# Optimization experiments

Hardware: AMD Instinct MI355X
Metric: run time of the kernel (lower is better)

## Reference

```python
import jax, jax.numpy as jnp
import numpy as np

N = 20000; E = 320000; IN = 128; OUT = 128; H = 8; D = 16
SQRT_DK = float(D) ** 0.5

def setup_inputs() -> dict:
    key = jax.random.key(0)
    ks = jax.random.split(key, 20)
    s = 0.05
    glorot = (6.0 / (D + D)) ** 0.5
    inp = dict(
        h_a=jax.random.normal(ks[0], (N, IN), jnp.float32),
        h_b=jax.random.normal(ks[1], (N, IN), jnp.float32),
        Wk=jax.random.normal(ks[2], (2, IN, OUT), jnp.float32) * s,
        bk=jnp.zeros((2, OUT), jnp.float32),
        Wq=jax.random.normal(ks[3], (2, IN, OUT), jnp.float32) * s,
        bq=jnp.zeros((2, OUT), jnp.float32),
        Wv=jax.random.normal(ks[4], (2, IN, OUT), jnp.float32) * s,
        bv=jnp.zeros((2, OUT), jnp.float32),
        Wa=jax.random.normal(ks[5], (2, OUT, OUT), jnp.float32) * s,
        ba=jnp.zeros((2, OUT), jnp.float32),
        rel_att=jax.random.normal(ks[6], (4, H, D, D), jnp.float32) * glorot,
        rel_msg=jax.random.normal(ks[7], (4, H, D, D), jnp.float32) * glorot,
        rel_pri=jnp.ones((4, H), jnp.float32),
        skip=jnp.ones((2,), jnp.float32),
    )
    names = ["src_aa", "dst_aa", "src_ab", "dst_ab", "src_ba", "dst_ba", "src_bb", "dst_bb"]
    for i, name in enumerate(names):
        inp[name] = jax.random.randint(ks[8 + i], (E,), 0, N, jnp.int32)
    return inp

def _relation(h_src, h_dst, src, dst, Wk_t, bk_t, Wq_t, bq_t, Wv_t, bv_t, att, msg, pri):
    # relation-specific K/V transform + Q projection
    k = (h_src @ Wk_t + bk_t).reshape(-1, H, D)
    v = (h_src @ Wv_t + bv_t).reshape(-1, H, D)
    q = (h_dst @ Wq_t + bq_t).reshape(-1, H, D)
    k = jnp.einsum('nhd,hde->nhe', k, att)
    v = jnp.einsum('nhd,hde->nhe', v, msg)
    # edge dot-product score (v_dot_u: q[dst] . k[src]), [E, H]
    score = jnp.einsum('ehd,ehd->eh', q[dst], k[src]) * pri / SQRT_DK
    # edge softmax normalized by dst
    smax = jax.ops.segment_max(score, dst, num_segments=N)
    ex = jnp.exp(score - smax[dst])
    ssum = jax.ops.segment_sum(ex, dst, num_segments=N)
    attn = ex / ssum[dst]
    # weighted scatter-aggregate, [N, H, D]
    return jax.ops.segment_sum(v[src] * attn[:, :, None], dst, num_segments=N)

def reference(h_a, h_b, Wk, bk, Wq, bq, Wv, bv, Wa, ba, rel_att, rel_msg, rel_pri, skip,
              src_aa, dst_aa, src_ab, dst_ab, src_ba, dst_ba, src_bb, dst_bb):
    agg_aa = _relation(h_a, h_a, src_aa, dst_aa, Wk[0], bk[0], Wq[0], bq[0], Wv[0], bv[0], rel_att[0], rel_msg[0], rel_pri[0])
    agg_ab = _relation(h_a, h_b, src_ab, dst_ab, Wk[0], bk[0], Wq[1], bq[1], Wv[0], bv[0], rel_att[1], rel_msg[1], rel_pri[1])
    agg_ba = _relation(h_b, h_a, src_ba, dst_ba, Wk[1], bk[1], Wq[0], bq[0], Wv[1], bv[1], rel_att[2], rel_msg[2], rel_pri[2])
    agg_bb = _relation(h_b, h_b, src_bb, dst_bb, Wk[1], bk[1], Wq[1], bq[1], Wv[1], bv[1], rel_att[3], rel_msg[3], rel_pri[3])
    # cross_reducer='mean' over the 2 relations targeting each node type
    t_a = (0.5 * (agg_aa + agg_ba)).reshape(N, OUT)
    t_b = (0.5 * (agg_ab + agg_bb)).reshape(N, OUT)
    al_a = jax.nn.sigmoid(skip[0])
    al_b = jax.nn.sigmoid(skip[1])
    new_a = al_a * (t_a @ Wa[0] + ba[0]) + (1.0 - al_a) * h_a
    new_b = al_b * (t_b @ Wa[1] + ba[1]) + (1.0 - al_b) * h_b
    return new_a, new_b
```

## Files before the change

kernel.cpp:

```cpp
#include <hip/hip_runtime.h>
#include <stdint.h>

#define N_NODES 20000
#define N_EDGES 320000
#define C 128
#define H 8
#define D 16
#define SLOT 64
#define NRANGE 5000
#define BUCKETS 2500
#define BCAP 224

#define P_CVT 2500
#define P_ZERO 157
#define P_PACK 128
#define P_FUSE 32
#define PB_EDGES 16384
#define PART_BLOCKS 80
#define PROJ_BLOCKS 3130
#define MB_TOTAL (PART_BLOCKS + PROJ_BLOCKS)

typedef short s16x8 __attribute__((ext_vector_type(8)));
typedef float f32x4 __attribute__((ext_vector_type(4)));

__device__ __forceinline__ unsigned short f2bf(float f) {
    unsigned int b = __float_as_uint(f);
    b += 0x7fffu + ((b >> 16) & 1u);
    return (unsigned short)(b >> 16);
}
__device__ __forceinline__ float bf2f(unsigned int u) {
    return __uint_as_float(u << 16);
}
__device__ __forceinline__ float bf_lo(unsigned int u) {
    return __uint_as_float(u << 16);
}
__device__ __forceinline__ float bf_hi(unsigned int u) {
    return __uint_as_float(u & 0xffff0000u);
}

__global__ __launch_bounds__(256) void prep_k(const float* __restrict__ h_a, const float* __restrict__ h_b,
                                              unsigned short* __restrict__ oa, unsigned short* __restrict__ ob,
                                              const float* __restrict__ Wq, const float* __restrict__ Wa,
                                              unsigned short* __restrict__ Wqt, unsigned short* __restrict__ Wat,
                                              const float* __restrict__ Wk, const float* __restrict__ Wv,
                                              const float* __restrict__ bk, const float* __restrict__ bv,
                                              const float* __restrict__ att, const float* __restrict__ msg,
                                              unsigned short* __restrict__ Wkt, unsigned short* __restrict__ Wvt,
                                              float* __restrict__ bkt, float* __restrict__ bvt,
                                              int* __restrict__ cur) {
    __shared__ float sa[D * D], sm[D * D];
    int bid = blockIdx.x;
    int tid = threadIdx.x;
    if (bid < P_CVT) {
        int i = (bid * 256 + tid) * 4;
        float4 va = *(const float4*)(h_a + i);
        float4 vb = *(const float4*)(h_b + i);
        ushort4 ua = { f2bf(va.x), f2bf(va.y), f2bf(va.z), f2bf(va.w) };
        ushort4 ub = { f2bf(vb.x), f2bf(vb.y), f2bf(vb.z), f2bf(vb.w) };
        *(ushort4*)(oa + i) = ua;
        *(ushort4*)(ob + i) = ub;
        return;
    }
    bid -= P_CVT;
    if (bid < P_ZERO) {
        int i = bid * 256 + tid;
        if (i < 40000) ((int4*)cur)[i] = make_int4(0, 0, 0, 0);
        return;
    }
    bid -= P_ZERO;
    if (bid < P_PACK) {
        int n = bid;
        int t = tid >> 7, i = tid & 127;
        Wqt[(t * C + n) * C + i] = f2bf(Wq[(t * C + i) * C + n]);
        Wat[(t * C + n) * C + i] = f2bf(Wa[(t * C + i) * C + n]);
        return;
    }
    bid -= P_PACK;
    {
        int r = bid >> 3, h = bid & 7;
        int t = r >> 1;
        if (tid < D * D) {
            sa[tid] = att[(r * H + h) * D * D + tid];
            sm[tid] = msg[(r * H + h) * D * D + tid];
        }
        __syncthreads();
        int i = tid & 127;
        for (int e = (tid >> 7); e < D; e += 2) {
            float sk = 0.f, sv = 0.f;
            for (int d = 0; d < D; ++d) {
                sk += Wk[(t * C + i) * C + h * D + d] * sa[d * D + e];
                sv += Wv[(t * C + i) * C + h * D + d] * sm[d * D + e];
            }
            Wkt[(r * C + h * D + e) * C + i] = f2bf(sk);
            Wvt[(r * C + h * D + e) * C + i] = f2bf(sv);
        }
        if (tid < D) {
            int e = tid;
            float sk = 0.f, sv = 0.f;
            for (int d = 0; d < D; ++d) {
                sk += bk[t * C + h * D + d] * sa[d * D + e];
                sv += bv[t * C + h * D + d] * sm[d * D + e];
            }
            bkt[r * C + h * D + e] = sk;
            bvt[r * C + h * D + e] = sv;
        }
    }
}

__global__ __launch_bounds__(256) void mega_k(const int* __restrict__ s0, const int* __restrict__ s1,
                                              const int* __restrict__ s2, const int* __restrict__ s3,
                                              const int* __restrict__ d0, const int* __restrict__ d1,
                                              const int* __restrict__ d2, const int* __restrict__ d3,
                                              int* __restrict__ cur, unsigned int* __restrict__ part,
                                              const unsigned short* __restrict__ ha,
                                              const unsigned short* __restrict__ hb,
                                              const unsigned short* __restrict__ Wqt,
                                              const unsigned short* __restrict__ Wkt,
                                              const unsigned short* __restrict__ Wvt,
                                              const float* __restrict__ bq,
                                              const float* __restrict__ bkt,
                                              const float* __restrict__ bvt,
                                              unsigned short* __restrict__ Qa,
                                              unsigned short* __restrict__ Qb,
                                              unsigned short* __restrict__ Kall,
                                              unsigned short* __restrict__ Vall) {
    __shared__ int hcnt[BUCKETS];
    __shared__ int hbase[BUCKETS];
    int bid = blockIdx.x;
    int tid = threadIdx.x;

    if (bid < PART_BLOCKS) {
        int r  = bid & 3;
        int pb = bid >> 2;
        int start = pb * PB_EDGES;
        int nval = N_EDGES - start;
        if (nval > PB_EDGES) nval = PB_EDGES;
        int nq = nval >> 2;
        const int* dd = (r == 0) ? d0 : (r == 1) ? d1 : (r == 2) ? d2 : d3;
        const int* ss = (r == 0) ? s0 : (r == 1) ? s1 : (r == 2) ? s2 : s3;
        for (int b = tid; b < BUCKETS; b += 256) hcnt[b] = 0;
        __syncthreads();
        for (int i = tid; i < nq; i += 256) {
            int4 d4 = *(const int4*)(dd + start + i * 4);
            atomicAdd(&hcnt[d4.x >> 3], 1);
            atomicAdd(&hcnt[d4.y >> 3], 1);
            atomicAdd(&hcnt[d4.z >> 3], 1);
            atomicAdd(&hcnt[d4.w >> 3], 1);
        }
        __syncthreads();
        for (int b = tid; b < BUCKETS; b += 256) {
            int c = hcnt[b];
            hbase[b] = c ? atomicAdd(&cur[(r * BUCKETS + b) * 16], c) : 0;
            hcnt[b] = 0;
        }
        __syncthreads();
        for (int i = tid; i < nq; i += 256) {
            int4 d4 = *(const int4*)(dd + start + i * 4);
            int4 s4 = *(const int4*)(ss + start + i * 4);
            int b0 = d4.x >> 3, b1 = d4.y >> 3, b2 = d4.z >> 3, b3 = d4.w >> 3;
            int i0 = atomicAdd(&hcnt[b0], 1);
            int i1 = atomicAdd(&hcnt[b1], 1);
            int i2 = atomicAdd(&hcnt[b2], 1);
            int i3 = atomicAdd(&hcnt[b3], 1);
            int p0 = hbase[b0] + i0, p1 = hbase[b1] + i1, p2 = hbase[b2] + i2, p3 = hbase[b3] + i3;
            if (p0 < BCAP) part[(size_t)(r * BUCKETS + b0) * BCAP + p0] = (unsigned int)s4.x | ((unsigned int)(d4.x & 7) << 15);
            if (p1 < BCAP) part[(size_t)(r * BUCKETS + b1) * BCAP + p1] = (unsigned int)s4.y | ((unsigned int)(d4.y & 7) << 15);
            if (p2 < BCAP) part[(size_t)(r * BUCKETS + b2) * BCAP + p2] = (unsigned int)s4.z | ((unsigned int)(d4.z & 7) << 15);
            if (p3 < BCAP) part[(size_t)(r * BUCKETS + b3) * BCAP + p3] = (unsigned int)s4.w | ((unsigned int)(d4.w & 7) << 15);
        }
        return;
    }
    int proj_id = bid - PART_BLOCKS;
    int j = proj_id / 313;
    int xb = proj_id - j * 313;
    const unsigned short* A;
    const unsigned short* Wt;
    const float* bias;
    unsigned short* Out;
    if (j < 2) {
        A = j ? hb : ha; Wt = Wqt + j * C * C; bias = bq + j * C; Out = j ? Qb : Qa;
    } else if (j < 6) {
        int r = j - 2;
        A = (r < 2) ? ha : hb; Wt = Wkt + r * C * C; bias = bkt + r * C;
        Out = Kall + (size_t)r * N_NODES * C;
    } else {
        int r = j - 6;
        A = (r < 2) ? ha : hb; Wt = Wvt + r * C * C; bias = bvt + r * C;
        Out = Vall + (size_t)r * N_NODES * C;
    }
    int wid = threadIdx.x >> 6, l = threadIdx.x & 63;
    int row_base = xb * 64 + wid * 16;
    int lm = l & 15, q = l >> 4;
    f32x4 acc[8] = {};
    int arow = row_base + lm;
    if (arow >= N_NODES) arow = N_NODES - 1;
    const s16x8* Ap = (const s16x8*)(A + (size_t)arow * C);
#pragma unroll
    for (int kc = 0; kc < 4; ++kc) {
        s16x8 af = Ap[kc * 4 + q];
#pragma unroll
        for (int t = 0; t < 8; ++t) {
            s16x8 bf = *(const s16x8*)(Wt + (t * 16 + lm) * C + kc * 32 + q * 8);
            acc[t] = __builtin_amdgcn_mfma_f32_16x16x32_bf16(af, bf, acc[t], 0, 0, 0);
        }
    }
#pragma unroll
    for (int t = 0; t < 8; ++t) {
        int col = t * 16 + lm;
        float b = bias[col];
#pragma unroll
        for (int i = 0; i < 4; ++i) {
            int row = row_base + q * 4 + i;
            if (row < N_NODES) Out[(size_t)row * C + col] = f2bf(acc[t][i] + b);
        }
    }
}

__global__ __launch_bounds__(256) void final_mm(const unsigned short* __restrict__ AggAll,
                                                const unsigned short* __restrict__ WatAll,
                                                const float* __restrict__ baAll,
                                                const float* __restrict__ skip,
                                                const float* __restrict__ h_a,
                                                const float* __restrict__ h_b,
                                                float* __restrict__ OutAll) {
    int ty = blockIdx.y;
    const unsigned short* Agg = AggAll + (size_t)ty * N_NODES * C;
    const unsigned short* Wat = WatAll + ty * C * C;
    const float* ba = baAll + ty * C;
    const float* h_orig = ty ? h_b : h_a;
    float* Out = OutAll + (size_t)ty * N_NODES * C;
    int wid = threadIdx.x >> 6, l = threadIdx.x & 63;
    int row_base = blockIdx.x * 64 + wid * 16;
    int lm = l & 15, q = l >> 4;
    f32x4 acc[8] = {};
    int arow = row_base + lm;
    if (arow >= N_NODES) arow = N_NODES - 1;
    const s16x8* Ap = (const s16x8*)(Agg + (size_t)arow * C);
#pragma unroll
    for (int kc = 0; kc < 4; ++kc) {
        s16x8 af = Ap[kc * 4 + q];
#pragma unroll
        for (int t = 0; t < 8; ++t) {
            s16x8 bf = *(const s16x8*)(Wat + (t * 16 + lm) * C + kc * 32 + q * 8);
            acc[t] = __builtin_amdgcn_mfma_f32_16x16x32_bf16(af, bf, acc[t], 0, 0, 0);
        }
    }
    float al = 1.f / (1.f + __expf(-skip[ty]));
#pragma unroll
    for (int t = 0; t < 8; ++t) {
        int col = t * 16 + lm;
        float b = ba[col];
#pragma unroll
        for (int i = 0; i < 4; ++i) {
            int row = row_base + q * 4 + i;
            if (row < N_NODES)
                Out[(size_t)row * C + col] = al * (acc[t][i] + b) + (1.f - al) * h_orig[(size_t)row * C + col];
        }
    }
}

__global__ __launch_bounds__(256) void node_p2(const int* __restrict__ cur,
                                               const unsigned int* __restrict__ part,
                                               const unsigned int* __restrict__ Kall,
                                               const unsigned int* __restrict__ Vall,
                                               const float* __restrict__ pri,
                                               const unsigned int* __restrict__ Qa,
                                               const unsigned int* __restrict__ Qb,
                                               unsigned int* __restrict__ agg) {
    __shared__ unsigned short slot[2][4][SLOT];
    __shared__ int cnt[2][4];
    int g = blockIdx.x;
    int xcd = g & 7, idx = g >> 3;
    int type = xcd >> 2;
    int range = (xcd & 3) * 1250 + idx;
    int relA = type ? 1 : 0;
    int relB = type ? 3 : 2;
    if (threadIdx.x < 8) ((int*)cnt)[threadIdx.x] = 0;
    __syncthreads();
    int bkt = range >> 1;
    int w   = range & 1;
#pragma unroll
    for (int rr = 0; rr < 2; ++rr) {
        int rel = rr ? relB : relA;
        int c = cur[(rel * BUCKETS + bkt) * 16];
        if (c > BCAP) c = BCAP;
        const unsigned int* pp = part + (size_t)(rel * BUCKETS + bkt) * BCAP;
        for (int i = threadIdx.x; i < c; i += 256) {
            unsigned int rec = pp[i];
            int dlow = (rec >> 15) & 7;
            if ((dlow >> 2) == w) {
                int dof = dlow & 3;
                int p = atomicAdd(&cnt[rr][dof], 1);
                if (p < SLOT) slot[rr][dof][p] = (unsigned short)(rec & 0x7fffu);
            }
        }
    }
    __syncthreads();

    int wid = threadIdx.x >> 6, l = threadIdx.x & 63;
    int eg = l >> 4;
    int j  = l & 15;
    int hg = j >> 1;
    int dof = wid;
    int n = range * 4 + dof;
    const unsigned int* Q32 = type ? Qb : Qa;
    uint4 qv = *(const uint4*)(Q32 + (size_t)n * 64 + j * 4);
    float q0 = bf_lo(qv.x), q1 = bf_hi(qv.x), q2 = bf_lo(qv.y), q3 = bf_hi(qv.y);
    float q4 = bf_lo(qv.z), q5 = bf_hi(qv.z), q6 = bf_lo(qv.w), q7 = bf_hi(qv.w);
    float out[8] = {};

#pragma unroll 1
    for (int rr = 0; rr < 2; ++rr) {
        int rel = rr ? relB : relA;
        const char* Kb = (const char*)(Kall + (size_t)rel * N_NODES * 64);
        const char* Vb = (const char*)(Vall + (size_t)rel * N_NODES * 64);
        float pv = pri[rel * 8 + hg] * 0.25f;
        int deg = cnt[rr][dof];
        if (deg > SLOT) deg = SLOT;
        float m = -1e30f, sum = 0.f;
        float acc[8] = {};
        for (int base = 0; base < deg; base += 16) {
            float s[4];
            uint4 vv[4];
#pragma unroll
            for (int i = 0; i < 4; ++i) {
                int idx2 = base + i * 4 + eg;
                float d = -1e30f;
                uint4 v = {0u, 0u, 0u, 0u};
                if (idx2 < deg) {
                    unsigned off = ((unsigned)slot[rr][dof][idx2] << 8) | ((unsigned)j << 4);
                    uint4 kv = *(const uint4*)(Kb + off);
                    v = *(const uint4*)(Vb + off);
                    d = q0 * bf_lo(kv.x) + q1 * bf_hi(kv.x)
                      + q2 * bf_lo(kv.y) + q3 * bf_hi(kv.y)
                      + q4 * bf_lo(kv.z) + q5 * bf_hi(kv.z)
                      + q6 * bf_lo(kv.w) + q7 * bf_hi(kv.w);
                    d += __shfl_xor(d, 1);
                    d *= pv;
                }
                s[i] = d;
                vv[i] = v;
            }
            float mloc = fmaxf(fmaxf(s[0], s[1]), fmaxf(s[2], s[3]));
            float mnew = fmaxf(m, mloc);
            float alpha = __expf(m - mnew);
            sum *= alpha;
#pragma unroll
            for (int c2 = 0; c2 < 8; ++c2) acc[c2] *= alpha;
            m = mnew;
#pragma unroll
            for (int i = 0; i < 4; ++i) {
                float ww = (s[i] > -1e29f) ? __expf(s[i] - m) : 0.f;
                sum += ww;
                acc[0] += ww * bf_lo(vv[i].x); acc[1] += ww * bf_hi(vv[i].x);
                acc[2] += ww * bf_lo(vv[i].y); acc[3] += ww * bf_hi(vv[i].y);
                acc[4] += ww * bf_lo(vv[i].z); acc[5] += ww * bf_hi(vv[i].z);
                acc[6] += ww * bf_lo(vv[i].w); acc[7] += ww * bf_hi(vv[i].w);
            }
        }
        float m1 = fmaxf(m, __shfl_xor(m, 16));
        float m2 = fmaxf(m1, __shfl_xor(m1, 32));
        float beta = __expf(m - m2);
        sum *= beta;
        sum += __shfl_xor(sum, 16);
        sum += __shfl_xor(sum, 32);
#pragma unroll
        for (int c2 = 0; c2 < 8; ++c2) {
            float a = acc[c2] * beta;
            a += __shfl_xor(a, 16);
            a += __shfl_xor(a, 32);
            acc[c2] = a;
        }
        if (deg > 0) {
            float rs = 1.f / sum;
#pragma unroll
            for (int c2 = 0; c2 < 8; ++c2) out[c2] += acc[c2] * rs;
        }
    }
    if (eg == 0) {
        uint4 pk;
        pk.x = (unsigned int)f2bf(0.5f * out[0]) | ((unsigned int)f2bf(0.5f * out[1]) << 16);
        pk.y = (unsigned int)f2bf(0.5f * out[2]) | ((unsigned int)f2bf(0.5f * out[3]) << 16);
        pk.z = (unsigned int)f2bf(0.5f * out[4]) | ((unsigned int)f2bf(0.5f * out[5]) << 16);
        pk.w = (unsigned int)f2bf(0.5f * out[6]) | ((unsigned int)f2bf(0.5f * out[7]) << 16);
        *(uint4*)(agg + ((size_t)type * N_NODES + n) * 64 + j * 4) = pk;
    }
}

extern "C" void kernel_launch(void* const* d_in, const int* in_sizes, int n_in,
                              void* d_out, int out_size, void* d_ws, size_t ws_size,
                              hipStream_t stream) {
    const float* h_a  = (const float*)d_in[0];
    const float* h_b  = (const float*)d_in[1];
    const float* Wk   = (const float*)d_in[2];
    const float* bk   = (const float*)d_in[3];
    const float* Wq   = (const float*)d_in[4];
    const float* bq   = (const float*)d_in[5];
    const float* Wv   = (const float*)d_in[6];
    const float* bv   = (const float*)d_in[7];
    const float* Wa   = (const float*)d_in[8];
    const float* ba   = (const float*)d_in[9];
    const float* att  = (const float*)d_in[10];
    const float* msg  = (const float*)d_in[11];
    const float* pri  = (const float*)d_in[12];
    const float* skip = (const float*)d_in[13];
    const int* srcs[4] = {(const int*)d_in[14], (const int*)d_in[16], (const int*)d_in[18], (const int*)d_in[20]};
    const int* dsts[4] = {(const int*)d_in[15], (const int*)d_in[17], (const int*)d_in[19], (const int*)d_in[21]};
    float* out = (float*)d_out;

    char* w = (char*)d_ws;
    auto alloc = [&](size_t bytes) {
        char* p = w;
        w += (bytes + 255) & ~(size_t)255;
        return p;
    };
    unsigned short* ha_bf = (unsigned short*)alloc((size_t)N_NODES * C * 2);
    unsigned short* hb_bf = (unsigned short*)alloc((size_t)N_NODES * C * 2);
    unsigned short* Qa    = (unsigned short*)alloc((size_t)N_NODES * C * 2);
    unsigned short* Qb    = (unsigned short*)alloc((size_t)N_NODES * C * 2);
    unsigned short* Kall  = (unsigned short*)alloc((size_t)4 * N_NODES * C * 2);
    unsigned short* Vall  = (unsigned short*)alloc((size_t)4 * N_NODES * C * 2);
    unsigned short* Wqt   = (unsigned short*)alloc(2 * C * C * 2);
    unsigned short* Wat   = (unsigned short*)alloc(2 * C * C * 2);
    unsigned short* Wkt   = (unsigned short*)alloc(4 * C * C * 2);
    unsigned short* Wvt   = (unsigned short*)alloc(4 * C * C * 2);
    float* bkt            = (float*)alloc(4 * C * 4);
    float* bvt            = (float*)alloc(4 * C * 4);
    int* cur              = (int*)alloc((size_t)4 * BUCKETS * 16 * 4);
    unsigned int* part    = (unsigned int*)alloc((size_t)4 * BUCKETS * BCAP * 4);
    unsigned short* agg   = (unsigned short*)alloc((size_t)2 * N_NODES * C * 2);

    prep_k<<<P_CVT + P_ZERO + P_PACK + P_FUSE, 256, 0, stream>>>(
        h_a, h_b, ha_bf, hb_bf, Wq, Wa, Wqt, Wat,
        Wk, Wv, bk, bv, att, msg, Wkt, Wvt, bkt, bvt, cur);

    mega_k<<<MB_TOTAL, 256, 0, stream>>>(
        srcs[0], srcs[1], srcs[2], srcs[3],
        dsts[0], dsts[1], dsts[2], dsts[3],
        cur, part,
        ha_bf, hb_bf, Wqt, Wkt, Wvt, bq, bkt, bvt,
        Qa, Qb, Kall, Vall);

    node_p2<<<2 * NRANGE, 256, 0, stream>>>(cur, part,
                                            (const unsigned int*)Kall, (const unsigned int*)Vall,
                                            pri,
                                            (const unsigned int*)Qa, (const unsigned int*)Qb,
                                            (unsigned int*)agg);

    final_mm<<<dim3(313, 2), 256, 0, stream>>>(agg, Wat, ba, skip, h_a, h_b, out);
}
```

Before: 307.7 us.

## Fuse final output projection and skip blend into node aggregation kernel

Removes the separate final_mm kernel and the bf16 aggregate buffer. Each node_p2 block keeps its four nodes' aggregated features in fp32 shared memory, then computes the Wa projection, bias, and sigmoid-weighted skip blend with scalar FMAs over bf16 weights. This saves a kernel launch and the aggregate round trip through global memory. In exchange, MFMA is replaced by scalar dot products, and each thread rereads 256-byte weight rows for every node.

```diff
diff --git a/kernel.cpp b/kernel.cpp
--- a/kernel.cpp
+++ b/kernel.cpp
@@ -216,49 +216,6 @@
     }
 }
 
-__global__ __launch_bounds__(256) void final_mm(const unsigned short* __restrict__ AggAll,
-                                                const unsigned short* __restrict__ WatAll,
-                                                const float* __restrict__ baAll,
-                                                const float* __restrict__ skip,
-                                                const float* __restrict__ h_a,
-                                                const float* __restrict__ h_b,
-                                                float* __restrict__ OutAll) {
-    int ty = blockIdx.y;
-    const unsigned short* Agg = AggAll + (size_t)ty * N_NODES * C;
-    const unsigned short* Wat = WatAll + ty * C * C;
-    const float* ba = baAll + ty * C;
-    const float* h_orig = ty ? h_b : h_a;
-    float* Out = OutAll + (size_t)ty * N_NODES * C;
-    int wid = threadIdx.x >> 6, l = threadIdx.x & 63;
-    int row_base = blockIdx.x * 64 + wid * 16;
-    int lm = l & 15, q = l >> 4;
-    f32x4 acc[8] = {};
-    int arow = row_base + lm;
-    if (arow >= N_NODES) arow = N_NODES - 1;
-    const s16x8* Ap = (const s16x8*)(Agg + (size_t)arow * C);
-#pragma unroll
-    for (int kc = 0; kc < 4; ++kc) {
-        s16x8 af = Ap[kc * 4 + q];
-#pragma unroll
-        for (int t = 0; t < 8; ++t) {
-            s16x8 bf = *(const s16x8*)(Wat + (t * 16 + lm) * C + kc * 32 + q * 8);
-            acc[t] = __builtin_amdgcn_mfma_f32_16x16x32_bf16(af, bf, acc[t], 0, 0, 0);
-        }
-    }
-    float al = 1.f / (1.f + __expf(-skip[ty]));
-#pragma unroll
-    for (int t = 0; t < 8; ++t) {
-        int col = t * 16 + lm;
-        float b = ba[col];
-#pragma unroll
-        for (int i = 0; i < 4; ++i) {
-            int row = row_base + q * 4 + i;
-            if (row < N_NODES)
-                Out[(size_t)row * C + col] = al * (acc[t][i] + b) + (1.f - al) * h_orig[(size_t)row * C + col];
-        }
-    }
-}
-
 __global__ __launch_bounds__(256) void node_p2(const int* __restrict__ cur,
                                                const unsigned int* __restrict__ part,
                                                const unsigned int* __restrict__ Kall,
@@ -266,9 +223,15 @@
                                                const float* __restrict__ pri,
                                                const unsigned int* __restrict__ Qa,
                                                const unsigned int* __restrict__ Qb,
-                                               unsigned int* __restrict__ agg) {
+                                               const unsigned short* __restrict__ WatAll,
+                                               const float* __restrict__ baAll,
+                                               const float* __restrict__ skip,
+                                               const float* __restrict__ h_a,
+                                               const float* __restrict__ h_b,
+                                               float* __restrict__ OutAll) {
     __shared__ unsigned short slot[2][4][SLOT];
     __shared__ int cnt[2][4];
+    __shared__ __align__(16) float aggl[4][C];
     int g = blockIdx.x;
     int xcd = g & 7, idx = g >> 3;
     int type = xcd >> 2;
@@ -378,12 +341,37 @@
         }
     }
     if (eg == 0) {
-        uint4 pk;
-        pk.x = (unsigned int)f2bf(0.5f * out[0]) | ((unsigned int)f2bf(0.5f * out[1]) << 16);
-        pk.y = (unsigned int)f2bf(0.5f * out[2]) | ((unsigned int)f2bf(0.5f * out[3]) << 16);
-        pk.z = (unsigned int)f2bf(0.5f * out[4]) | ((unsigned int)f2bf(0.5f * out[5]) << 16);
-        pk.w = (unsigned int)f2bf(0.5f * out[6]) | ((unsigned int)f2bf(0.5f * out[7]) << 16);
-        *(uint4*)(agg + ((size_t)type * N_NODES + n) * 64 + j * 4) = pk;
+#pragma unroll
+        for (int c2 = 0; c2 < 8; ++c2) aggl[dof][j * 8 + c2] = 0.5f * out[c2];
+    }
+    __syncthreads();
+    {
+        const unsigned short* Wt = WatAll + type * C * C;
+        const float* bat = baAll + type * C;
+        const float* horig = type ? h_b : h_a;
+        float* Outp = OutAll + (size_t)type * N_NODES * C;
+        float al = 1.f / (1.f + __expf(-skip[type]));
+#pragma unroll
+        for (int it = 0; it < 2; ++it) {
+            int e = it * 256 + threadIdx.x;
+            int nd = e >> 7, col = e & 127;
+            int node = range * 4 + nd;
+            const uint4* w4 = (const uint4*)(Wt + (size_t)col * C);
+            const float4* ag4 = (const float4*)aggl[nd];
+            float acc = 0.f;
+#pragma unroll
+            for (int kc = 0; kc < 16; ++kc) {
+                uint4 wv = w4[kc];
+                float4 a0 = ag4[kc * 2];
+                float4 a1 = ag4[kc * 2 + 1];
+                acc += a0.x * bf_lo(wv.x) + a0.y * bf_hi(wv.x)
+                     + a0.z * bf_lo(wv.y) + a0.w * bf_hi(wv.y)
+                     + a1.x * bf_lo(wv.z) + a1.y * bf_hi(wv.z)
+                     + a1.z * bf_lo(wv.w) + a1.w * bf_hi(wv.w);
+            }
+            Outp[(size_t)node * C + col] =
+                al * (acc + bat[col]) + (1.f - al) * horig[(size_t)node * C + col];
+        }
     }
 }
 
@@ -428,7 +416,6 @@
     float* bvt            = (float*)alloc(4 * C * 4);
     int* cur              = (int*)alloc((size_t)4 * BUCKETS * 16 * 4);
     unsigned int* part    = (unsigned int*)alloc((size_t)4 * BUCKETS * BCAP * 4);
-    unsigned short* agg   = (unsigned short*)alloc((size_t)2 * N_NODES * C * 2);
 
     prep_k<<<P_CVT + P_ZERO + P_PACK + P_FUSE, 256, 0, stream>>>(
         h_a, h_b, ha_bf, hb_bf, Wq, Wa, Wqt, Wat,
@@ -445,7 +432,5 @@
                                             (const unsigned int*)Kall, (const unsigned int*)Vall,
                                             pri,
                                             (const unsigned int*)Qa, (const unsigned int*)Qb,
-                                            (unsigned int*)agg);
-
-    final_mm<<<dim3(313, 2), 256, 0, stream>>>(agg, Wat, ba, skip, h_a, h_b, out);
-}
+                                            Wat, ba, skip, h_a, h_b, out);
+}
```

Result: slower. 555.4 us (+80.5%).
